# Kernel tuning notes

Measured on AMD Instinct MI355X. Metric: run time of the kernel, lower is better.

The kernel has to match this reference:

```python
import jax, jax.numpy as jnp
import numpy as np

EMBED_DIM = 1024
NUM_HEADS = 16
HEAD_DIM = EMBED_DIM // NUM_HEADS
SCALE = 1.0 / np.sqrt(HEAD_DIM)


def _quant_linear(x, w, b):
    # Per-tensor symmetric int8 quantize -> dequantize -> GEMM (faithful to QuantizedLinear)
    s = jnp.max(jnp.abs(w)) / 127.0
    w_dq = jnp.clip(jnp.round(w / s), -128.0, 127.0) * s
    return jnp.einsum('bse,oe->bso', x, w_dq) + b


def setup_inputs() -> dict:
    key = jax.random.key(0)
    ks = jax.random.split(key, 7)
    B, S, E = 2, 2048, EMBED_DIM
    return {
        'query': jax.random.normal(ks[0], (B, S, E), dtype=jnp.float32),
        'key': jax.random.normal(ks[1], (B, S, E), dtype=jnp.float32),
        'value': jax.random.normal(ks[2], (B, S, E), dtype=jnp.float32),
        'Wq': jax.random.normal(ks[3], (E, E), dtype=jnp.float32) * 0.02,
        'bq': jnp.zeros((E,), dtype=jnp.float32),
        'Wk': jax.random.normal(ks[4], (E, E), dtype=jnp.float32) * 0.02,
        'bk': jnp.zeros((E,), dtype=jnp.float32),
        'Wv': jax.random.normal(ks[5], (E, E), dtype=jnp.float32) * 0.02,
        'bv': jnp.zeros((E,), dtype=jnp.float32),
        'Wo': jax.random.normal(ks[6], (E, E), dtype=jnp.float32) * 0.02,
        'bo': jnp.zeros((E,), dtype=jnp.float32),
    }


def reference(query, key, value, Wq, bq, Wk, bk, Wv, bv, Wo, bo):
    B, S, E = query.shape
    H, D = NUM_HEADS, HEAD_DIM
    Q = _quant_linear(query, Wq, bq).reshape(B, S, H, D).transpose(0, 2, 1, 3)
    K = _quant_linear(key, Wk, bk).reshape(B, S, H, D).transpose(0, 2, 1, 3)
    V = _quant_linear(value, Wv, bv).reshape(B, S, H, D).transpose(0, 2, 1, 3)
    # [B,H,S,S] unfused attention scores
    scores = jnp.einsum('bhqd,bhkd->bhqk', Q, K) * SCALE
    attn = jax.nn.softmax(scores, axis=-1)  # dropout is identity at inference
    out = jnp.einsum('bhqk,bhkd->bhqd', attn, V)
    out = out.transpose(0, 2, 1, 3).reshape(B, S, E)
    return _quant_linear(out, Wo, bo)
```

## Files before the change

### kernel.cpp

```cpp
#include <hip/hip_runtime.h>
#include <math.h>

#define S_LEN 2048
#define EMB   1024
#define NHEAD 16
#define HDIM  64
#define MTOT  4096
#define EXP2_SCALE 0.18033688011112042f

typedef __attribute__((ext_vector_type(8))) short bf16x8;
typedef __attribute__((ext_vector_type(4))) float f32x4;

#if __has_builtin(__builtin_amdgcn_exp2f)
#define FEXP2(x) __builtin_amdgcn_exp2f(x)
#else
#define FEXP2(x) exp2f(x)
#endif

__device__ __forceinline__ short f2bf(float f) {
  union { float f; unsigned u; } v; v.f = f;
  unsigned r = v.u + 0x7fffu + ((v.u >> 16) & 1u);
  return (short)(r >> 16);
}
__device__ __forceinline__ float bf2f(short s) {
  union { float f; unsigned u; } v; v.u = ((unsigned)(unsigned short)s) << 16;
  return v.f;
}
__device__ __forceinline__ unsigned pkbf(float e0, float e1) {
  unsigned a = __float_as_uint(e1) + 0x8000u;
  unsigned b = __float_as_uint(e0) + 0x8000u;
  return __builtin_amdgcn_perm(a, b, 0x07060302u);
}

__device__ __forceinline__ void gload_lds16(const void* g, void* l) {
  __builtin_amdgcn_global_load_lds(
      (const __attribute__((address_space(1))) void*)g,
      (__attribute__((address_space(3))) void*)l, 16, 0, 0);
}

__global__ void wabsmax_k(const float* __restrict__ W0, const float* __restrict__ W1,
                          const float* __restrict__ W2, const float* __restrict__ W3,
                          unsigned* __restrict__ scaleU) {
  int w = blockIdx.x & 3;
  int part = blockIdx.x >> 2;
  const float* W = (w == 0) ? W0 : (w == 1) ? W1 : (w == 2) ? W2 : W3;
  float m = 0.f;
  int base = part * 16384;
#pragma unroll
  for (int p = 0; p < 16; ++p) {
    const float4 v = *(const float4*)&W[base + p * 1024 + threadIdx.x * 4];
    m = fmaxf(m, fmaxf(fmaxf(fabsf(v.x), fabsf(v.y)), fmaxf(fabsf(v.z), fabsf(v.w))));
  }
  __shared__ float red[256];
  red[threadIdx.x] = m;
  __syncthreads();
  for (int s = 128; s > 0; s >>= 1) {
    if (threadIdx.x < s) red[threadIdx.x] = fmaxf(red[threadIdx.x], red[threadIdx.x + s]);
    __syncthreads();
  }
  if (threadIdx.x == 0) atomicMax(&scaleU[w], __float_as_uint(red[0]));
}

__global__ void wquant_k(const float* __restrict__ W0, const float* __restrict__ W1,
                         const float* __restrict__ W2, const float* __restrict__ W3,
                         short* __restrict__ Q0, short* __restrict__ Q1,
                         short* __restrict__ Q2, short* __restrict__ Q3,
                         const unsigned* __restrict__ scaleU, float* __restrict__ sVal) {
  int w = blockIdx.y;
  const float* W = (w == 0) ? W0 : (w == 1) ? W1 : (w == 2) ? W2 : W3;
  short* Q = (w == 0) ? Q0 : (w == 1) ? Q1 : (w == 2) ? Q2 : Q3;
  float s = __uint_as_float(scaleU[w]) * (1.0f / 127.0f);
  if (blockIdx.x == 0 && threadIdx.x == 0) sVal[w] = s;
  int idx = (blockIdx.x * 256 + threadIdx.x) * 4;
  float4 v = *(const float4*)&W[idx];
  short4 q;
  q.x = f2bf(fminf(fmaxf(rintf(v.x / s), -128.f), 127.f));
  q.y = f2bf(fminf(fmaxf(rintf(v.y / s), -128.f), 127.f));
  q.z = f2bf(fminf(fmaxf(rintf(v.z / s), -128.f), 127.f));
  q.w = f2bf(fminf(fmaxf(rintf(v.w / s), -128.f), 127.f));
  *(short4*)&Q[idx] = q;
}

__global__ void acast_k(const float* __restrict__ A0, const float* __restrict__ A1,
                        const float* __restrict__ A2,
                        short* __restrict__ H0, short* __restrict__ H1,
                        short* __restrict__ H2) {
  int w = blockIdx.y;
  const float* A = (w == 0) ? A0 : (w == 1) ? A1 : A2;
  short* H = (w == 0) ? H0 : (w == 1) ? H1 : H2;
  int idx = (blockIdx.x * 256 + threadIdx.x) * 4;
  float4 v = *(const float4*)&A[idx];
  short4 h;
  h.x = f2bf(v.x); h.y = f2bf(v.y); h.z = f2bf(v.z); h.w = f2bf(v.w);
  *(short4*)&H[idx] = h;
}

__device__ __forceinline__ void gemm_core(
    const short* __restrict__ Ah, const short* __restrict__ Bq, int m0, int n0,
    short* AhS, short* BsS, f32x4 acc[4][4]) {
  const int tid = threadIdx.x;
  const int lane = tid & 63, wave = tid >> 6;
  const int quad = lane >> 4, l16 = lane & 15;
  const int wm = wave >> 1, wn = wave & 1;

  const int swrow = lane >> 2, swcol = (lane & 3) * 8;
  const short* agh = Ah + (m0 + wave * 32 + swrow) * 1024 + swcol;
  const short* bgp = Bq + (n0 + wave * 32 + swrow) * 1024 + swcol;
  short* sA0 = AhS + wave * 1024;
  short* sB0 = BsS + wave * 1024;

  for (int k0 = 0; k0 < 1024; k0 += 32) {
    __syncthreads();
    gload_lds16(agh + k0,             sA0);
    gload_lds16(agh + 16 * 1024 + k0, sA0 + 512);
    gload_lds16(bgp + k0,             sB0);
    gload_lds16(bgp + 16 * 1024 + k0, sB0 + 512);
    __syncthreads();
    bf16x8 ah[4], bb[4];
#pragma unroll
    for (int mi = 0; mi < 4; ++mi) {
      int row = wm * 64 + mi * 16 + l16;
      ah[mi] = *(const bf16x8*)&AhS[row * 32 + quad * 8];
    }
#pragma unroll
    for (int ni = 0; ni < 4; ++ni) {
      int row = wn * 64 + ni * 16 + l16;
      bb[ni] = *(const bf16x8*)&BsS[row * 32 + quad * 8];
    }
#pragma unroll
    for (int mi = 0; mi < 4; ++mi)
#pragma unroll
      for (int ni = 0; ni < 4; ++ni)
        acc[mi][ni] = __builtin_amdgcn_mfma_f32_16x16x32_bf16(ah[mi], bb[ni], acc[mi][ni], 0, 0, 0);
  }
}

__global__ __launch_bounds__(256, 2) void gemm_qkv(
    const short* __restrict__ QA, const short* __restrict__ KA, const short* __restrict__ VA,
    const short* __restrict__ WqQ, const short* __restrict__ WkQ, const short* __restrict__ WvQ,
    const float* __restrict__ sVal,
    const float* __restrict__ bq, const float* __restrict__ bk, const float* __restrict__ bv,
    short* __restrict__ Qh, short* __restrict__ Kh, short* __restrict__ Vh) {
  __shared__ __align__(16) short AhS[128 * 32];
  __shared__ __align__(16) short BsS[128 * 32];
  const int z = blockIdx.z;
  const short* Ah = (z == 0) ? QA : (z == 1) ? KA : VA;
  const short* Bq = (z == 0) ? WqQ : (z == 1) ? WkQ : WvQ;
  const float* bias = (z == 0) ? bq : (z == 1) ? bk : bv;
  short* oh = (z == 0) ? Qh : (z == 1) ? Kh : Vh;

  const int lin = blockIdx.y * 8 + blockIdx.x;
  const int map = (lin & 7) * 32 + (lin >> 3);
  const int m0 = (map >> 3) * 128, n0 = (map & 7) * 128;
  f32x4 acc[4][4];
#pragma unroll
  for (int i = 0; i < 4; ++i)
#pragma unroll
    for (int j = 0; j < 4; ++j) acc[i][j] = (f32x4){0.f, 0.f, 0.f, 0.f};

  gemm_core(Ah, Bq, m0, n0, AhS, BsS, acc);

  const int lane = threadIdx.x & 63, wave = threadIdx.x >> 6;
  const int quad = lane >> 4, l16 = lane & 15;
  const int wm = wave >> 1, wn = wave & 1;
  float s = sVal[z];
  float post = (z == 0) ? EXP2_SCALE : 1.0f;
#pragma unroll
  for (int mi = 0; mi < 4; ++mi) {
#pragma unroll
    for (int ni = 0; ni < 4; ++ni) {
      int rowb = m0 + wm * 64 + mi * 16 + quad * 4;
      int col = n0 + wn * 64 + ni * 16 + l16;
      float bia = bias[col];
      int h = col >> 6, d = col & 63;
      if (z < 2) {
#pragma unroll
        for (int r = 0; r < 4; ++r) {
          float v = (acc[mi][ni][r] * s + bia) * post;
          int row = rowb + r;
          int b = row >> 11, sq = row & 2047;
          oh[((b * 16 + h) * 2048 + sq) * 64 + d] = f2bf(v);
        }
      } else {
        int b = rowb >> 11, sq = rowb & 2047;
        short4 pk;
        pk.x = f2bf(acc[mi][ni][0] * s + bia);
        pk.y = f2bf(acc[mi][ni][1] * s + bia);
        pk.z = f2bf(acc[mi][ni][2] * s + bia);
        pk.w = f2bf(acc[mi][ni][3] * s + bia);
        *(short4*)&oh[((b * 16 + h) * 64 + d) * 2048 + sq] = pk;
      }
    }
  }
}

__global__ __launch_bounds__(256, 2) void gemm_o(
    const short* __restrict__ OAh, const short* __restrict__ OAl,
    const short* __restrict__ WoQ, const float* __restrict__ sPtr,
    const float* __restrict__ bias, float* __restrict__ outF) {
  __shared__ __align__(16) short AhS[128 * 32];
  __shared__ __align__(16) short AlS[128 * 32];
  __shared__ __align__(16) short BsS[64 * 32];
  const int tid = threadIdx.x;
  const int lane = tid & 63, wave = tid >> 6;
  const int quad = lane >> 4, l16 = lane & 15;
  const int lin = blockIdx.y * 16 + blockIdx.x;
  const int map = (lin & 7) * 64 + (lin >> 3);
  const int m0 = (map >> 4) * 128, n0 = (map & 15) * 64;

  f32x4 acc[2][4];
#pragma unroll
  for (int i = 0; i < 2; ++i)
#pragma unroll
    for (int j = 0; j < 4; ++j) acc[i][j] = (f32x4){0.f, 0.f, 0.f, 0.f};

  const int swrow = lane >> 2, swcol = (lane & 3) * 8;
  const short* agh = OAh + (m0 + wave * 32 + swrow) * 1024 + swcol;
  const short* agl = OAl + (m0 + wave * 32 + swrow) * 1024 + swcol;
  const short* bgp = WoQ + (n0 + wave * 16 + swrow) * 1024 + swcol;
  short* sA0 = AhS + wave * 1024;
  short* sA1 = AlS + wave * 1024;
  short* sB0 = BsS + wave * 512;

  for (int k0 = 0; k0 < 1024; k0 += 32) {
    __syncthreads();
    gload_lds16(agh + k0,             sA0);
    gload_lds16(agh + 16 * 1024 + k0, sA0 + 512);
    gload_lds16(agl + k0,             sA1);
    gload_lds16(agl + 16 * 1024 + k0, sA1 + 512);
    gload_lds16(bgp + k0,             sB0);
    __syncthreads();
    bf16x8 ah[2], al[2], bb[4];
#pragma unroll
    for (int mi = 0; mi < 2; ++mi) {
      int row = wave * 32 + mi * 16 + l16;
      ah[mi] = *(const bf16x8*)&AhS[row * 32 + quad * 8];
      al[mi] = *(const bf16x8*)&AlS[row * 32 + quad * 8];
    }
#pragma unroll
    for (int ni = 0; ni < 4; ++ni) {
      int row = ni * 16 + l16;
      bb[ni] = *(const bf16x8*)&BsS[row * 32 + quad * 8];
    }
#pragma unroll
    for (int mi = 0; mi < 2; ++mi)
#pragma unroll
      for (int ni = 0; ni < 4; ++ni) {
        acc[mi][ni] = __builtin_amdgcn_mfma_f32_16x16x32_bf16(ah[mi], bb[ni], acc[mi][ni], 0, 0, 0);
        acc[mi][ni] = __builtin_amdgcn_mfma_f32_16x16x32_bf16(al[mi], bb[ni], acc[mi][ni], 0, 0, 0);
      }
  }

  const float s = *sPtr;
#pragma unroll
  for (int mi = 0; mi < 2; ++mi) {
#pragma unroll
    for (int ni = 0; ni < 4; ++ni) {
      int rowb = m0 + wave * 32 + mi * 16 + quad * 4;
      int col = n0 + ni * 16 + l16;
      float bia = bias[col];
#pragma unroll
      for (int r = 0; r < 4; ++r)
        outF[(rowb + r) * 1024 + col] = acc[mi][ni][r] * s + bia;
    }
  }
}

#define MF(a, b, c) __builtin_amdgcn_mfma_f32_16x16x32_bf16(a, b, c, 0, 0, 0)

#define FLASH_TILE(KF, KN, ktv)                                               \
  {                                                                           \
    __syncthreads();                                                          \
    *(bf16x8*)&Vhs[vOff]      = pv0;                                          \
    *(bf16x8*)&Vhs[vOff + 32] = pv1;                                          \
    __syncthreads();                                                          \
    const int ktn = (ktv) + 64;                                               \
    if (ktn < S_LEN) {                                                        \
      pv0 = *(const bf16x8*)&Vh[vgl + ktn];                                   \
      pv1 = *(const bf16x8*)&Vh[vgl + ktn + 32];                              \
      const int ko = ktn * HDIM;                                              \
      KN##0 = *(const bf16x8*)&kp0[ko]; KN##1 = *(const bf16x8*)&kp0[ko + 32];\
      KN##2 = *(const bf16x8*)&kp1[ko]; KN##3 = *(const bf16x8*)&kp1[ko + 32];\
      KN##4 = *(const bf16x8*)&kp2[ko]; KN##5 = *(const bf16x8*)&kp2[ko + 32];\
      KN##6 = *(const bf16x8*)&kp3[ko]; KN##7 = *(const bf16x8*)&kp3[ko + 32];\
    }                                                                         \
    f32x4 sc[2][4];                                                           \
    {                                                                         \
      f32x4 sv;                                                               \
      sv = zero; sv = MF(KF##0, qb[0][0], sv); sv = MF(KF##1, qb[0][1], sv);  \
      sc[0][0] = sv;                                                          \
      sv = zero; sv = MF(KF##0, qb[1][0], sv); sv = MF(KF##1, qb[1][1], sv);  \
      sc[1][0] = sv;                                                          \
      sv = zero; sv = MF(KF##2, qb[0][0], sv); sv = MF(KF##3, qb[0][1], sv);  \
      sc[0][1] = sv;                                                          \
      sv = zero; sv = MF(KF##2, qb[1][0], sv); sv = MF(KF##3, qb[1][1], sv);  \
      sc[1][1] = sv;                                                          \
      sv = zero; sv = MF(KF##4, qb[0][0], sv); sv = MF(KF##5, qb[0][1], sv);  \
      sc[0][2] = sv;                                                          \
      sv = zero; sv = MF(KF##4, qb[1][0], sv); sv = MF(KF##5, qb[1][1], sv);  \
      sc[1][2] = sv;                                                          \
      sv = zero; sv = MF(KF##6, qb[0][0], sv); sv = MF(KF##7, qb[0][1], sv);  \
      sc[0][3] = sv;                                                          \
      sv = zero; sv = MF(KF##6, qb[1][0], sv); sv = MF(KF##7, qb[1][1], sv);  \
      sc[1][3] = sv;                                                          \
    }                                                                         \
    _Pragma("unroll")                                                         \
    for (int g = 0; g < 2; ++g)                                               \
      _Pragma("unroll")                                                       \
      for (int nj = 0; nj < 4; ++nj)                                          \
        _Pragma("unroll")                                                     \
        for (int r = 0; r < 4; ++r)                                           \
          sc[g][nj][r] = FEXP2(sc[g][nj][r]);                                 \
    union { bf16x8 v; unsigned u[4]; } P[2][2];                               \
    _Pragma("unroll")                                                         \
    for (int g = 0; g < 2; ++g) {                                             \
      P[g][0].u[0] = pkbf(sc[g][0][0], sc[g][0][1]);                          \
      P[g][0].u[1] = pkbf(sc[g][0][2], sc[g][0][3]);                          \
      P[g][0].u[2] = pkbf(sc[g][1][0], sc[g][1][1]);                          \
      P[g][0].u[3] = pkbf(sc[g][1][2], sc[g][1][3]);                          \
      P[g][1].u[0] = pkbf(sc[g][2][0], sc[g][2][1]);                          \
      P[g][1].u[1] = pkbf(sc[g][2][2], sc[g][2][3]);                          \
      P[g][1].u[2] = pkbf(sc[g][3][0], sc[g][3][1]);                          \
      P[g][1].u[3] = pkbf(sc[g][3][2], sc[g][3][3]);                          \
    }                                                                         \
    _Pragma("unroll")                                                         \
    for (int g = 0; g < 2; ++g) {                                             \
      sacc[g] = MF(P[g][0].v, ones_.v, sacc[g]);                              \
      sacc[g] = MF(P[g][1].v, ones_.v, sacc[g]);                              \
    }                                                                         \
    _Pragma("unroll")                                                         \
    for (int ni = 0; ni < 4; ++ni) {                                          \
      int vr = ni * 16 + l16;                                                 \
      bf16x8 vf0 = *(const bf16x8*)&Vhs[vr * 72 + quad * 8];                  \
      bf16x8 vf1 = *(const bf16x8*)&Vhs[vr * 72 + 32 + quad * 8];             \
      _Pragma("unroll")                                                       \
      for (int g = 0; g < 2; ++g) {                                           \
        oacc[g][ni] = MF(P[g][0].v, vf0, oacc[g][ni]);                        \
        oacc[g][ni] = MF(P[g][1].v, vf1, oacc[g][ni]);                        \
      }                                                                       \
    }                                                                         \
  }

__global__ __launch_bounds__(256, 2) void flash_k(
    const short* __restrict__ Qh, const short* __restrict__ Kh,
    const short* __restrict__ Vh,
    short* __restrict__ Ohi, short* __restrict__ Olo) {
  __shared__ __align__(16) short Vhs[64 * 72];

  const int tid = threadIdx.x;
  const int lane = tid & 63, wave = tid >> 6;
  const int quad = lane >> 4, l16 = lane & 15;
  const int lin = blockIdx.y * 16 + blockIdx.x;
  const int map = (lin & 7) * 64 + (lin >> 3);
  const int bh = map >> 4;
  const int b = bh >> 4, h = bh & 15;
  const int q0 = (map & 15) * 128 + wave * 32;
  const int qkbase = bh * (S_LEN * HDIM);
  const int vbase  = bh * (HDIM * S_LEN);

  bf16x8 qb[2][2];
#pragma unroll
  for (int g = 0; g < 2; ++g) {
    const int qrow = qkbase + (q0 + g * 16 + l16) * HDIM;
    qb[g][0] = *(const bf16x8*)&Qh[qrow + quad * 8];
    qb[g][1] = *(const bf16x8*)&Qh[qrow + 32 + quad * 8];
  }

  f32x4 zero = {0.f, 0.f, 0.f, 0.f};
  f32x4 oacc[2][4];
#pragma unroll
  for (int g = 0; g < 2; ++g)
#pragma unroll
    for (int i = 0; i < 4; ++i) oacc[g][i] = zero;
  f32x4 sacc[2] = {zero, zero};

  union { bf16x8 v; unsigned u[4]; } ones_;
  ones_.u[0] = ones_.u[1] = ones_.u[2] = ones_.u[3] = 0x3F803F80u;

  const int sr  = wave * 16 + l16;
  const int sc8 = quad * 8;
  const int vgl  = vbase + sr * S_LEN + sc8;
  const int vOff = sr * 72 + sc8;

  const int rbase = (l16 & 3) | ((l16 & 12) << 1);
  const short* kp0 = Kh + qkbase + (rbase | 0 ) * HDIM + quad * 8;
  const short* kp1 = Kh + qkbase + (rbase | 4 ) * HDIM + quad * 8;
  const short* kp2 = Kh + qkbase + (rbase | 32) * HDIM + quad * 8;
  const short* kp3 = Kh + qkbase + (rbase | 36) * HDIM + quad * 8;

  bf16x8 pv0 = *(const bf16x8*)&Vh[vgl];
  bf16x8 pv1 = *(const bf16x8*)&Vh[vgl + 32];
  bf16x8 kA0 = *(const bf16x8*)&kp0[0], kA1 = *(const bf16x8*)&kp0[32];
  bf16x8 kA2 = *(const bf16x8*)&kp1[0], kA3 = *(const bf16x8*)&kp1[32];
  bf16x8 kA4 = *(const bf16x8*)&kp2[0], kA5 = *(const bf16x8*)&kp2[32];
  bf16x8 kA6 = *(const bf16x8*)&kp3[0], kA7 = *(const bf16x8*)&kp3[32];
  bf16x8 kB0 = kA0, kB1 = kA1, kB2 = kA2, kB3 = kA3;
  bf16x8 kB4 = kA4, kB5 = kA5, kB6 = kA6, kB7 = kA7;

  for (int kt = 0; kt < S_LEN; kt += 128) {
    FLASH_TILE(kA, kB, kt)
    FLASH_TILE(kB, kA, kt + 64)
  }
#pragma unroll
  for (int g = 0; g < 2; ++g) {
#pragma unroll
    for (int r = 0; r < 4; ++r) {
      float inv = 1.f / sacc[g][r];
      int row = b * S_LEN + q0 + g * 16 + quad * 4 + r;
#pragma unroll
      for (int ni = 0; ni < 4; ++ni) {
        float v = oacc[g][ni][r] * inv;
        int idx = row * 1024 + h * 64 + ni * 16 + l16;
        short hi = f2bf(v);
        Ohi[idx] = hi;
        Olo[idx] = f2bf(v - bf2f(hi));
      }
    }
  }
}

extern "C" void kernel_launch(void* const* d_in, const int* in_sizes, int n_in,
                              void* d_out, int out_size, void* d_ws, size_t ws_size,
                              hipStream_t stream) {
  const float* query = (const float*)d_in[0];
  const float* key_i = (const float*)d_in[1];
  const float* value = (const float*)d_in[2];
  const float* Wq = (const float*)d_in[3];
  const float* bq = (const float*)d_in[4];
  const float* Wk = (const float*)d_in[5];
  const float* bk = (const float*)d_in[6];
  const float* Wv = (const float*)d_in[7];
  const float* bv = (const float*)d_in[8];
  const float* Wo = (const float*)d_in[9];
  const float* bo = (const float*)d_in[10];
  float* out = (float*)d_out;

  char* w = (char*)d_ws;
  unsigned* scaleU = (unsigned*)w;
  float* sVal = (float*)(w + 256);
  size_t off = 512;
  const size_t SZ_W = 2097152;
  const size_t SZ_A = 8388608;
  short* WqQ = (short*)(w + off); off += SZ_W;
  short* WkQ = (short*)(w + off); off += SZ_W;
  short* WvQ = (short*)(w + off); off += SZ_W;
  short* WoQ = (short*)(w + off); off += SZ_W;
  short* Qa  = (short*)(w + off); off += SZ_A;
  short* Ka  = (short*)(w + off); off += SZ_A;
  short* Va  = (short*)(w + off); off += SZ_A;
  short* Qh  = (short*)(w + off); off += SZ_A;
  short* Kh  = (short*)(w + off); off += SZ_A;
  short* Vh  = (short*)(w + off); off += SZ_A;
  short* Ohi = Qa;
  short* Olo = Ka;

  (void)hipMemsetAsync(scaleU, 0, 16, stream);
  wabsmax_k<<<256, 256, 0, stream>>>(Wq, Wk, Wv, Wo, scaleU);
  wquant_k<<<dim3(1024, 4), 256, 0, stream>>>(Wq, Wk, Wv, Wo, WqQ, WkQ, WvQ, WoQ, scaleU, sVal);
  acast_k<<<dim3(4096, 3), 256, 0, stream>>>(query, key_i, value, Qa, Ka, Va);
  gemm_qkv<<<dim3(8, 32, 3), 256, 0, stream>>>(Qa, Ka, Va, WqQ, WkQ, WvQ, sVal,
                                               bq, bk, bv, Qh, Kh, Vh);
  flash_k<<<dim3(16, 32), 256, 0, stream>>>(Qh, Kh, Vh, Ohi, Olo);
  gemm_o<<<dim3(16, 32), 256, 0, stream>>>(Ohi, Olo, WoQ, sVal + 3, bo, out);
}
```

Measured before the change: 270.0 us.

## Stage K through double-buffered LDS and halve barriers in flash loop

K tiles are now loaded cooperatively once per block into shared memory, using a row permutation that keeps the MFMA operand order. Previously each wave loaded its own 8 K fragments from global memory. K and V use ping-pong LDS buffers, so one barrier per 64-key tile replaces two, and the next tile's global loads overlap the current compute. This cuts redundant global K traffic and registers, at the cost of more LDS (4 buffers) and extra LDS reads per tile.

```diff
diff --git a/kernel.cpp b/kernel.cpp
--- a/kernel.cpp
+++ b/kernel.cpp
@@ -266,43 +266,21 @@
   }
 }
 
-#define MF(a, b, c) __builtin_amdgcn_mfma_f32_16x16x32_bf16(a, b, c, 0, 0, 0)
-
-#define FLASH_TILE(KF, KN, ktv)                                               \
+#define FLASH_COMPUTE(Kbuf, Vbuf)                                             \
   {                                                                           \
-    __syncthreads();                                                          \
-    *(bf16x8*)&Vhs[vOff]      = pv0;                                          \
-    *(bf16x8*)&Vhs[vOff + 32] = pv1;                                          \
-    __syncthreads();                                                          \
-    const int ktn = (ktv) + 64;                                               \
-    if (ktn < S_LEN) {                                                        \
-      pv0 = *(const bf16x8*)&Vh[vgl + ktn];                                   \
-      pv1 = *(const bf16x8*)&Vh[vgl + ktn + 32];                              \
-      const int ko = ktn * HDIM;                                              \
-      KN##0 = *(const bf16x8*)&kp0[ko]; KN##1 = *(const bf16x8*)&kp0[ko + 32];\
-      KN##2 = *(const bf16x8*)&kp1[ko]; KN##3 = *(const bf16x8*)&kp1[ko + 32];\
-      KN##4 = *(const bf16x8*)&kp2[ko]; KN##5 = *(const bf16x8*)&kp2[ko + 32];\
-      KN##6 = *(const bf16x8*)&kp3[ko]; KN##7 = *(const bf16x8*)&kp3[ko + 32];\
-    }                                                                         \
     f32x4 sc[2][4];                                                           \
-    {                                                                         \
-      f32x4 sv;                                                               \
-      sv = zero; sv = MF(KF##0, qb[0][0], sv); sv = MF(KF##1, qb[0][1], sv);  \
-      sc[0][0] = sv;                                                          \
-      sv = zero; sv = MF(KF##0, qb[1][0], sv); sv = MF(KF##1, qb[1][1], sv);  \
-      sc[1][0] = sv;                                                          \
-      sv = zero; sv = MF(KF##2, qb[0][0], sv); sv = MF(KF##3, qb[0][1], sv);  \
-      sc[0][1] = sv;                                                          \
-      sv = zero; sv = MF(KF##2, qb[1][0], sv); sv = MF(KF##3, qb[1][1], sv);  \
-      sc[1][1] = sv;                                                          \
-      sv = zero; sv = MF(KF##4, qb[0][0], sv); sv = MF(KF##5, qb[0][1], sv);  \
-      sc[0][2] = sv;                                                          \
-      sv = zero; sv = MF(KF##4, qb[1][0], sv); sv = MF(KF##5, qb[1][1], sv);  \
-      sc[1][2] = sv;                                                          \
-      sv = zero; sv = MF(KF##6, qb[0][0], sv); sv = MF(KF##7, qb[0][1], sv);  \
-      sc[0][3] = sv;                                                          \
-      sv = zero; sv = MF(KF##6, qb[1][0], sv); sv = MF(KF##7, qb[1][1], sv);  \
-      sc[1][3] = sv;                                                          \
+    _Pragma("unroll")                                                         \
+    for (int nj = 0; nj < 4; ++nj) {                                          \
+      const int kr = nj * 16 + l16;                                           \
+      bf16x8 kf0 = *(const bf16x8*)&Kbuf[kr * 72 + quad * 8];                 \
+      bf16x8 kf1 = *(const bf16x8*)&Kbuf[kr * 72 + 32 + quad * 8];            \
+      _Pragma("unroll")                                                       \
+      for (int g = 0; g < 2; ++g) {                                           \
+        f32x4 sv = zero;                                                      \
+        sv = __builtin_amdgcn_mfma_f32_16x16x32_bf16(kf0, qb[g][0], sv, 0, 0, 0); \
+        sv = __builtin_amdgcn_mfma_f32_16x16x32_bf16(kf1, qb[g][1], sv, 0, 0, 0); \
+        sc[g][nj] = sv;                                                       \
+      }                                                                       \
     }                                                                         \
     _Pragma("unroll")                                                         \
     for (int g = 0; g < 2; ++g)                                               \
@@ -325,27 +303,46 @@
     }                                                                         \
     _Pragma("unroll")                                                         \
     for (int g = 0; g < 2; ++g) {                                             \
-      sacc[g] = MF(P[g][0].v, ones_.v, sacc[g]);                              \
-      sacc[g] = MF(P[g][1].v, ones_.v, sacc[g]);                              \
+      sacc[g] = __builtin_amdgcn_mfma_f32_16x16x32_bf16(P[g][0].v, ones_.v, sacc[g], 0, 0, 0); \
+      sacc[g] = __builtin_amdgcn_mfma_f32_16x16x32_bf16(P[g][1].v, ones_.v, sacc[g], 0, 0, 0); \
     }                                                                         \
     _Pragma("unroll")                                                         \
     for (int ni = 0; ni < 4; ++ni) {                                          \
       int vr = ni * 16 + l16;                                                 \
-      bf16x8 vf0 = *(const bf16x8*)&Vhs[vr * 72 + quad * 8];                  \
-      bf16x8 vf1 = *(const bf16x8*)&Vhs[vr * 72 + 32 + quad * 8];             \
+      bf16x8 vf0 = *(const bf16x8*)&Vbuf[vr * 72 + quad * 8];                 \
+      bf16x8 vf1 = *(const bf16x8*)&Vbuf[vr * 72 + 32 + quad * 8];            \
       _Pragma("unroll")                                                       \
       for (int g = 0; g < 2; ++g) {                                           \
-        oacc[g][ni] = MF(P[g][0].v, vf0, oacc[g][ni]);                        \
-        oacc[g][ni] = MF(P[g][1].v, vf1, oacc[g][ni]);                        \
+        oacc[g][ni] = __builtin_amdgcn_mfma_f32_16x16x32_bf16(P[g][0].v, vf0, oacc[g][ni], 0, 0, 0); \
+        oacc[g][ni] = __builtin_amdgcn_mfma_f32_16x16x32_bf16(P[g][1].v, vf1, oacc[g][ni], 0, 0, 0); \
       }                                                                       \
     }                                                                         \
+  }
+
+#define FLASH_STORE(Kbuf, Vbuf)                                               \
+  {                                                                           \
+    *(bf16x8*)&Kbuf[kOff]      = pk0;                                         \
+    *(bf16x8*)&Kbuf[kOff + 32] = pk1;                                         \
+    *(bf16x8*)&Vbuf[vOff]      = pv0;                                         \
+    *(bf16x8*)&Vbuf[vOff + 32] = pv1;                                         \
+  }
+
+#define FLASH_LOAD(ktn)                                                       \
+  {                                                                           \
+    pk0 = *(const bf16x8*)&Kh[kgl + (ktn) * HDIM];                            \
+    pk1 = *(const bf16x8*)&Kh[kgl + (ktn) * HDIM + 32];                       \
+    pv0 = *(const bf16x8*)&Vh[vgl + (ktn)];                                   \
+    pv1 = *(const bf16x8*)&Vh[vgl + (ktn) + 32];                              \
   }
 
 __global__ __launch_bounds__(256, 2) void flash_k(
     const short* __restrict__ Qh, const short* __restrict__ Kh,
     const short* __restrict__ Vh,
     short* __restrict__ Ohi, short* __restrict__ Olo) {
-  __shared__ __align__(16) short Vhs[64 * 72];
+  __shared__ __align__(16) short KhsA[64 * 72];
+  __shared__ __align__(16) short VhsA[64 * 72];
+  __shared__ __align__(16) short KhsB[64 * 72];
+  __shared__ __align__(16) short VhsB[64 * 72];
 
   const int tid = threadIdx.x;
   const int lane = tid & 63, wave = tid >> 6;
@@ -379,27 +376,26 @@
 
   const int sr  = wave * 16 + l16;
   const int sc8 = quad * 8;
-  const int vgl  = vbase + sr * S_LEN + sc8;
+  const int srP = (sr & 32) | (((sr >> 2) & 1) << 4) | (((sr >> 3) & 3) << 2) | (sr & 3);
+  const int kgl = qkbase + sr * HDIM + sc8;
+  const int vgl = vbase + sr * S_LEN + sc8;
+  const int kOff = srP * 72 + sc8;
   const int vOff = sr * 72 + sc8;
 
-  const int rbase = (l16 & 3) | ((l16 & 12) << 1);
-  const short* kp0 = Kh + qkbase + (rbase | 0 ) * HDIM + quad * 8;
-  const short* kp1 = Kh + qkbase + (rbase | 4 ) * HDIM + quad * 8;
-  const short* kp2 = Kh + qkbase + (rbase | 32) * HDIM + quad * 8;
-  const short* kp3 = Kh + qkbase + (rbase | 36) * HDIM + quad * 8;
-
-  bf16x8 pv0 = *(const bf16x8*)&Vh[vgl];
-  bf16x8 pv1 = *(const bf16x8*)&Vh[vgl + 32];
-  bf16x8 kA0 = *(const bf16x8*)&kp0[0], kA1 = *(const bf16x8*)&kp0[32];
-  bf16x8 kA2 = *(const bf16x8*)&kp1[0], kA3 = *(const bf16x8*)&kp1[32];
-  bf16x8 kA4 = *(const bf16x8*)&kp2[0], kA5 = *(const bf16x8*)&kp2[32];
-  bf16x8 kA6 = *(const bf16x8*)&kp3[0], kA7 = *(const bf16x8*)&kp3[32];
-  bf16x8 kB0 = kA0, kB1 = kA1, kB2 = kA2, kB3 = kA3;
-  bf16x8 kB4 = kA4, kB5 = kA5, kB6 = kA6, kB7 = kA7;
+  bf16x8 pk0, pk1, pv0, pv1;
+  FLASH_LOAD(0)
+  FLASH_STORE(KhsA, VhsA)
 
   for (int kt = 0; kt < S_LEN; kt += 128) {
-    FLASH_TILE(kA, kB, kt)
-    FLASH_TILE(kB, kA, kt + 64)
+    __syncthreads();
+    FLASH_LOAD(kt + 64)
+    FLASH_COMPUTE(KhsA, VhsA)
+    FLASH_STORE(KhsB, VhsB)
+    __syncthreads();
+    const bool more = (kt + 128 < S_LEN);
+    if (more) FLASH_LOAD(kt + 128)
+    FLASH_COMPUTE(KhsB, VhsB)
+    if (more) FLASH_STORE(KhsA, VhsA)
   }
 #pragma unroll
   for (int g = 0; g < 2; ++g) {
```

Result: faster. 236.8 us (-12.3%).
